# Kernel tuning notes

Hardware: AMD Instinct MI355X
Metric: run time of the kernel (lower is better)

The kernel has to match this reference:

```python
import jax, jax.numpy as jnp
import numpy as np

ALPHA = 0.2  # LeakyReLU negative slope
B, L, FIN, FOUT = 128, 512, 128, 128

def setup_inputs() -> dict:
    key = jax.random.key(0)
    k1, k2, k3, k4, k5 = jax.random.split(key, 5)
    h = jax.random.normal(k1, (B, L, FIN), jnp.float32)
    W = jax.random.normal(k2, (FIN, FOUT), jnp.float32) * (1.0 / np.sqrt(FIN))
    a = jax.random.normal(k3, (2 * FOUT,), jnp.float32) * (1.0 / np.sqrt(2 * FOUT))
    edge_bias = jax.random.normal(k4, (B, L, L), jnp.float32) * 0.1
    adj_mask = jax.random.uniform(k5, (L, L)) > 0.3
    adj_mask = adj_mask | jnp.eye(L, dtype=bool)  # self-loops avoid fully-masked rows
    return {"h": h, "W": W, "a": a, "edge_bias": edge_bias, "adj_mask": adj_mask}

def reference(h, W, a, edge_bias, adj_mask):
    # Wh: [B, L, Fout]
    Wh = jnp.einsum('blf,fo->blo', h, W)
    Fout = W.shape[1]
    # a([Wh_i, Wh_j]) == Wh_i @ a[:Fout] + Wh_j @ a[Fout:]  (avoids O(B*L*L*2F) concat)
    ei = Wh @ a[:Fout]   # [B, L]  (target i contribution)
    ej = Wh @ a[Fout:]   # [B, L]  (source j contribution)
    e = jax.nn.leaky_relu(ei[:, :, None] + ej[:, None, :], ALPHA) + edge_bias  # [B, L, L]
    e = jnp.where(adj_mask[None, :, :], e, -jnp.inf)
    att = jax.nn.softmax(e, axis=-1)  # dropout=0.0 -> identity
    h_prime = jnp.einsum('bij,bjo->bio', att, Wh)  # [B, L, Fout]
    return jax.nn.elu(h_prime)  # concat=True branch
```

## Files before the change

### kernel.cpp

```cpp
#include <hip/hip_runtime.h>
#include <string.h>

#define ALPHA 0.2f

typedef short short8 __attribute__((ext_vector_type(8)));
typedef float floatx4 __attribute__((ext_vector_type(4)));
typedef int intx4 __attribute__((ext_vector_type(4)));
typedef unsigned short ushort4v __attribute__((ext_vector_type(4)));

__device__ inline unsigned short f2bf(float f) {
    unsigned int v; __builtin_memcpy(&v, &f, 4);
    v = v + 0x7FFFu + ((v >> 16) & 1u);
    return (unsigned short)(v >> 16);
}

__global__ __launch_bounds__(256) void wh_kernel(const float* __restrict__ h,
                                                 const float* __restrict__ W,
                                                 const float* __restrict__ a,
                                                 unsigned short* __restrict__ wht,
                                                 float* __restrict__ ei,
                                                 float* __restrict__ ej)
{
    __shared__ __align__(16) unsigned short h_s[128][136];
    __shared__ __align__(16) unsigned short w_s[128][136];
    __shared__ float a_s[256];
    const int tid  = threadIdx.x;
    const int lane = tid & 63;
    const int wv   = tid >> 6;
    const int quad = lane >> 4;
    const int l16  = lane & 15;
    const int r0   = blockIdx.x * 128;
    const int b    = r0 >> 9;
    const int jb   = r0 & 511;

    const float* hbase = h + (size_t)r0 * 128;
    for (int it = 0; it < 16; ++it) {
        int idx4 = it * 256 + tid;
        floatx4 v = *(const floatx4*)(hbase + idx4 * 4);
        int row = idx4 >> 5;
        int col = (idx4 & 31) * 4;
        ushort4v u;
        for (int e = 0; e < 4; ++e) u[e] = f2bf(v[e]);
        *(ushort4v*)&h_s[row][col] = u;
    }
    for (int it = 0; it < 64; ++it) {
        int idx = it * 256 + tid;
        w_s[idx & 127][idx >> 7] = f2bf(W[idx]);
    }
    a_s[tid] = a[tid];
    __syncthreads();

    floatx4 acc[8][2];
    for (int mo = 0; mo < 8; ++mo)
        for (int n = 0; n < 2; ++n) acc[mo][n] = (floatx4)0.f;

    for (int kk = 0; kk < 4; ++kk) {
        short8 bfr[2];
        for (int n = 0; n < 2; ++n)
            bfr[n] = *(const short8*)&h_s[wv * 32 + n * 16 + l16][kk * 32 + quad * 8];
        for (int mo = 0; mo < 8; ++mo) {
            short8 afr = *(const short8*)&w_s[mo * 16 + l16][kk * 32 + quad * 8];
            acc[mo][0] = __builtin_amdgcn_mfma_f32_16x16x32_bf16(afr, bfr[0], acc[mo][0], 0, 0, 0);
            acc[mo][1] = __builtin_amdgcn_mfma_f32_16x16x32_bf16(afr, bfr[1], acc[mo][1], 0, 0, 0);
        }
    }

    for (int n = 0; n < 2; ++n) {
        float si = 0.f, sj = 0.f;
        for (int mo = 0; mo < 8; ++mo)
            for (int r = 0; r < 4; ++r) {
                int o = mo * 16 + quad * 4 + r;
                float v = acc[mo][n][r];
                si += v * a_s[o];
                sj += v * a_s[128 + o];
            }
        si += __shfl_xor(si, 16); si += __shfl_xor(si, 32);
        sj += __shfl_xor(sj, 16); sj += __shfl_xor(sj, 32);
        if (quad == 0) {
            int j = jb + wv * 32 + n * 16 + l16;
            ei[b * 512 + j] = si;
            ej[b * 512 + j] = sj;
        }
    }

    for (int mo = 0; mo < 8; ++mo)
        for (int n = 0; n < 2; ++n)
            for (int r = 0; r < 4; ++r) {
                int o = mo * 16 + quad * 4 + r;
                int j = jb + wv * 32 + n * 16 + l16;
                wht[(size_t)b * 65536 + o * 512 + j] = f2bf(acc[mo][n][r]);
            }
}

__global__ __launch_bounds__(256, 4) void attn_kernel(const unsigned short* __restrict__ wht,
                                                      const float* __restrict__ ei,
                                                      const float* __restrict__ ej,
                                                      const float* __restrict__ bias,
                                                      const int* __restrict__ adj,
                                                      float* __restrict__ out)
{
    __shared__ __align__(16) unsigned short p_s[32][520];
    __shared__ float ei_s[32];
    __shared__ float s_row[32];

    const int tid  = threadIdx.x;
    const int lane = tid & 63;
    const int wv   = tid >> 6;
    const int quad = lane >> 4;
    const int l16  = lane & 15;
    const int b    = blockIdx.x >> 4;
    const int i0   = (blockIdx.x & 15) * 32;

    const floatx4 ejv0 = *(const floatx4*)(ej + b * 512 + lane * 4);
    const floatx4 ejv1 = *(const floatx4*)(ej + b * 512 + 256 + lane * 4);
    if (tid < 32) ei_s[tid] = ei[b * 512 + i0 + tid];
    __syncthreads();

    const float* bp = bias + ((size_t)(b * 512 + i0 + wv * 8)) * 512;
    const int*   ap = adj + (i0 + wv * 8) * 512;
    floatx4 bb0 = *(const floatx4*)(bp + lane * 4);
    floatx4 bb1 = *(const floatx4*)(bp + 256 + lane * 4);
    intx4   mm0 = *(const intx4*)(ap + lane * 4);
    intx4   mm1 = *(const intx4*)(ap + 256 + lane * 4);

    float rsum[8];

#pragma unroll
    for (int rr = 0; rr < 8; ++rr) {
        floatx4 nb0, nb1; intx4 nm0, nm1;
        if (rr < 7) {
            nb0 = *(const floatx4*)(bp + 512 + lane * 4);
            nb1 = *(const floatx4*)(bp + 768 + lane * 4);
            nm0 = *(const intx4*)(ap + 512 + lane * 4);
            nm1 = *(const intx4*)(ap + 768 + lane * 4);
        }
        const int il = wv * 8 + rr;
        const float eiv = ei_s[il];
        float sm = 0.f;
        ushort4v p0, p1;
        for (int e = 0; e < 4; ++e) {
            float x = eiv + ejv0[e];
            x = fmaxf(x, ALPHA * x);
            x += bb0[e];
            float p = __expf(x);
            p = (mm0[e] != 0) ? p : 0.f;
            sm += p;
            p0[e] = f2bf(p);
        }
        for (int e = 0; e < 4; ++e) {
            float x = eiv + ejv1[e];
            x = fmaxf(x, ALPHA * x);
            x += bb1[e];
            float p = __expf(x);
            p = (mm1[e] != 0) ? p : 0.f;
            sm += p;
            p1[e] = f2bf(p);
        }
        *(ushort4v*)&p_s[il][lane * 4]       = p0;
        *(ushort4v*)&p_s[il][256 + lane * 4] = p1;
        rsum[rr] = sm;
        bb0 = nb0; bb1 = nb1; mm0 = nm0; mm1 = nm1;
        bp += 512; ap += 512;
    }

#pragma unroll
    for (int rr = 0; rr < 8; ++rr)
        for (int off = 32; off; off >>= 1)
            rsum[rr] += __shfl_xor(rsum[rr], off);
    if (lane == 0)
#pragma unroll
        for (int rr = 0; rr < 8; ++rr) s_row[wv * 8 + rr] = rsum[rr];
    __syncthreads();

    floatx4 acc[2][2];
    for (int m = 0; m < 2; ++m)
        for (int n = 0; n < 2; ++n) acc[m][n] = (floatx4)0.f;

    const unsigned short* wbase = wht + (size_t)b * 65536;
    const unsigned short* wb0 = wbase + (wv * 32 + l16) * 512 + quad * 8;
    const unsigned short* wb1 = wbase + (wv * 32 + 16 + l16) * 512 + quad * 8;
    short8 bf0 = *(const short8*)(wb0);
    short8 bf1 = *(const short8*)(wb1);
#pragma unroll
    for (int k16 = 0; k16 < 16; ++k16) {
        int ko = k16 * 32 + quad * 8;
        short8 nbf0, nbf1;
        if (k16 < 15) {
            nbf0 = *(const short8*)(wb0 + (k16 + 1) * 32);
            nbf1 = *(const short8*)(wb1 + (k16 + 1) * 32);
        }
        short8 af0 = *(const short8*)&p_s[l16][ko];
        short8 af1 = *(const short8*)&p_s[16 + l16][ko];
        acc[0][0] = __builtin_amdgcn_mfma_f32_16x16x32_bf16(af0, bf0, acc[0][0], 0, 0, 0);
        acc[0][1] = __builtin_amdgcn_mfma_f32_16x16x32_bf16(af0, bf1, acc[0][1], 0, 0, 0);
        acc[1][0] = __builtin_amdgcn_mfma_f32_16x16x32_bf16(af1, bf0, acc[1][0], 0, 0, 0);
        acc[1][1] = __builtin_amdgcn_mfma_f32_16x16x32_bf16(af1, bf1, acc[1][1], 0, 0, 0);
        bf0 = nbf0; bf1 = nbf1;
    }

    for (int m = 0; m < 2; ++m)
        for (int n = 0; n < 2; ++n)
            for (int r = 0; r < 4; ++r) {
                int il = m * 16 + quad * 4 + r;
                int o  = wv * 32 + n * 16 + l16;
                float v = acc[m][n][r] / s_row[il];
                v = v > 0.f ? v : (__expf(v) - 1.f);
                out[((size_t)(b * 512 + i0 + il)) * 128 + o] = v;
            }
}

extern "C" void kernel_launch(void* const* d_in, const int* in_sizes, int n_in,
                              void* d_out, int out_size, void* d_ws, size_t ws_size,
                              hipStream_t stream)
{
    const float* h    = (const float*)d_in[0];
    const float* W    = (const float*)d_in[1];
    const float* a    = (const float*)d_in[2];
    const float* bias = (const float*)d_in[3];
    const int*   adj  = (const int*)d_in[4];
    float*       out  = (float*)d_out;

    unsigned short* wht = (unsigned short*)d_ws;
    float* ei = (float*)((char*)d_ws + 16777216);
    float* ej = ei + 65536;

    hipLaunchKernelGGL(wh_kernel,   dim3(512),  dim3(256), 0, stream, h, W, a, wht, ei, ej);
    hipLaunchKernelGGL(attn_kernel, dim3(2048), dim3(256), 0, stream, wht, ei, ej, bias, adj, out);
}
```

Baseline: 262.3 us.

## Halve attention row tile, precompute bf16 mask, deepen Wh prefetch

Adds a small kernel that converts the int adjacency mask into a bf16 0/1 multiplier once per call, halving the mask bytes read by the attention kernel and replacing the select with a multiply. The attention kernel now processes 16 rows per block instead of 32, doubling the grid. It issues all bias and mask loads up front and prefetches Wh four k-steps ahead. The cost is that each Wh tile is now reloaded by twice as many blocks, plus an extra launch.

```diff
diff --git a/kernel.cpp b/kernel.cpp
--- a/kernel.cpp
+++ b/kernel.cpp
@@ -12,6 +12,13 @@
     unsigned int v; __builtin_memcpy(&v, &f, 4);
     v = v + 0x7FFFu + ((v >> 16) & 1u);
     return (unsigned short)(v >> 16);
+}
+
+__global__ __launch_bounds__(256) void mask_kernel(const int* __restrict__ adj,
+                                                   unsigned short* __restrict__ mbf)
+{
+    int idx = blockIdx.x * 256 + threadIdx.x;
+    mbf[idx] = adj[idx] ? (unsigned short)0x3F80 : (unsigned short)0;
 }
 
 __global__ __launch_bounds__(256) void wh_kernel(const float* __restrict__ h,
@@ -92,121 +99,117 @@
             }
 }
 
-__global__ __launch_bounds__(256, 4) void attn_kernel(const unsigned short* __restrict__ wht,
-                                                      const float* __restrict__ ei,
-                                                      const float* __restrict__ ej,
-                                                      const float* __restrict__ bias,
-                                                      const int* __restrict__ adj,
-                                                      float* __restrict__ out)
-{
-    __shared__ __align__(16) unsigned short p_s[32][520];
-    __shared__ float ei_s[32];
-    __shared__ float s_row[32];
+__global__ __launch_bounds__(256) void attn_kernel(const unsigned short* __restrict__ wht,
+                                                   const float* __restrict__ ei,
+                                                   const float* __restrict__ ej,
+                                                   const float* __restrict__ bias,
+                                                   const unsigned short* __restrict__ mbf,
+                                                   float* __restrict__ out)
+{
+    __shared__ __align__(16) unsigned short p_s[16][520];
+    __shared__ float ei_s[16];
+    __shared__ float s_row[16];
 
     const int tid  = threadIdx.x;
     const int lane = tid & 63;
     const int wv   = tid >> 6;
     const int quad = lane >> 4;
     const int l16  = lane & 15;
-    const int b    = blockIdx.x >> 4;
-    const int i0   = (blockIdx.x & 15) * 32;
-
+    const int b    = blockIdx.x >> 5;
+    const int i0   = (blockIdx.x & 31) * 16;
+
+    const float* bp = bias + ((size_t)(b * 512 + i0 + wv * 4)) * 512;
+    const unsigned short* mp = mbf + (i0 + wv * 4) * 512;
+    floatx4 b0[4], b1[4];
+    ushort4v m0[4], m1[4];
+#pragma unroll
+    for (int r = 0; r < 4; ++r) {
+        b0[r] = *(const floatx4*)(bp + r * 512 + lane * 4);
+        b1[r] = *(const floatx4*)(bp + r * 512 + 256 + lane * 4);
+        m0[r] = *(const ushort4v*)(mp + r * 512 + lane * 4);
+        m1[r] = *(const ushort4v*)(mp + r * 512 + 256 + lane * 4);
+    }
     const floatx4 ejv0 = *(const floatx4*)(ej + b * 512 + lane * 4);
     const floatx4 ejv1 = *(const floatx4*)(ej + b * 512 + 256 + lane * 4);
-    if (tid < 32) ei_s[tid] = ei[b * 512 + i0 + tid];
+    if (tid < 16) ei_s[tid] = ei[b * 512 + i0 + tid];
+
+    const unsigned short* wb0 = wht + (size_t)b * 65536 + (wv * 32 + l16) * 512 + quad * 8;
+    const unsigned short* wb1 = wb0 + 16 * 512;
+    short8 pb0[4], pb1[4];
+#pragma unroll
+    for (int s = 0; s < 4; ++s) {
+        pb0[s] = *(const short8*)(wb0 + s * 32);
+        pb1[s] = *(const short8*)(wb1 + s * 32);
+    }
     __syncthreads();
 
-    const float* bp = bias + ((size_t)(b * 512 + i0 + wv * 8)) * 512;
-    const int*   ap = adj + (i0 + wv * 8) * 512;
-    floatx4 bb0 = *(const floatx4*)(bp + lane * 4);
-    floatx4 bb1 = *(const floatx4*)(bp + 256 + lane * 4);
-    intx4   mm0 = *(const intx4*)(ap + lane * 4);
-    intx4   mm1 = *(const intx4*)(ap + 256 + lane * 4);
-
-    float rsum[8];
-
-#pragma unroll
-    for (int rr = 0; rr < 8; ++rr) {
-        floatx4 nb0, nb1; intx4 nm0, nm1;
-        if (rr < 7) {
-            nb0 = *(const floatx4*)(bp + 512 + lane * 4);
-            nb1 = *(const floatx4*)(bp + 768 + lane * 4);
-            nm0 = *(const intx4*)(ap + 512 + lane * 4);
-            nm1 = *(const intx4*)(ap + 768 + lane * 4);
-        }
-        const int il = wv * 8 + rr;
+    float rsum[4];
+#pragma unroll
+    for (int r = 0; r < 4; ++r) {
+        const int il = wv * 4 + r;
         const float eiv = ei_s[il];
-        float sm = 0.f;
-        ushort4v p0, p1;
+        float p[8];
+#pragma unroll
         for (int e = 0; e < 4; ++e) {
             float x = eiv + ejv0[e];
             x = fmaxf(x, ALPHA * x);
-            x += bb0[e];
-            float p = __expf(x);
-            p = (mm0[e] != 0) ? p : 0.f;
-            sm += p;
-            p0[e] = f2bf(p);
-        }
+            x += b0[r][e];
+            float mlt; { unsigned int mv = ((unsigned int)m0[r][e]) << 16; __builtin_memcpy(&mlt, &mv, 4); }
+            p[e] = __expf(x) * mlt;
+        }
+#pragma unroll
         for (int e = 0; e < 4; ++e) {
             float x = eiv + ejv1[e];
             x = fmaxf(x, ALPHA * x);
-            x += bb1[e];
-            float p = __expf(x);
-            p = (mm1[e] != 0) ? p : 0.f;
-            sm += p;
-            p1[e] = f2bf(p);
-        }
-        *(ushort4v*)&p_s[il][lane * 4]       = p0;
-        *(ushort4v*)&p_s[il][256 + lane * 4] = p1;
-        rsum[rr] = sm;
-        bb0 = nb0; bb1 = nb1; mm0 = nm0; mm1 = nm1;
-        bp += 512; ap += 512;
-    }
-
-#pragma unroll
-    for (int rr = 0; rr < 8; ++rr)
+            x += b1[r][e];
+            float mlt; { unsigned int mv = ((unsigned int)m1[r][e]) << 16; __builtin_memcpy(&mlt, &mv, 4); }
+            p[4 + e] = __expf(x) * mlt;
+        }
+        float sm = 0.f;
+#pragma unroll
+        for (int e = 0; e < 8; ++e) sm += p[e];
+        rsum[r] = sm;
+        ushort4v pk0, pk1;
+        for (int e = 0; e < 4; ++e) pk0[e] = f2bf(p[e]);
+        for (int e = 0; e < 4; ++e) pk1[e] = f2bf(p[4 + e]);
+        *(ushort4v*)&p_s[il][lane * 4]       = pk0;
+        *(ushort4v*)&p_s[il][256 + lane * 4] = pk1;
+    }
+#pragma unroll
+    for (int r = 0; r < 4; ++r)
         for (int off = 32; off; off >>= 1)
-            rsum[rr] += __shfl_xor(rsum[rr], off);
+            rsum[r] += __shfl_xor(rsum[r], off);
     if (lane == 0)
 #pragma unroll
-        for (int rr = 0; rr < 8; ++rr) s_row[wv * 8 + rr] = rsum[rr];
+        for (int r = 0; r < 4; ++r) s_row[wv * 4 + r] = rsum[r];
     __syncthreads();
 
-    floatx4 acc[2][2];
-    for (int m = 0; m < 2; ++m)
-        for (int n = 0; n < 2; ++n) acc[m][n] = (floatx4)0.f;
-
-    const unsigned short* wbase = wht + (size_t)b * 65536;
-    const unsigned short* wb0 = wbase + (wv * 32 + l16) * 512 + quad * 8;
-    const unsigned short* wb1 = wbase + (wv * 32 + 16 + l16) * 512 + quad * 8;
-    short8 bf0 = *(const short8*)(wb0);
-    short8 bf1 = *(const short8*)(wb1);
+    floatx4 acc0 = (floatx4)0.f, acc1 = (floatx4)0.f;
 #pragma unroll
     for (int k16 = 0; k16 < 16; ++k16) {
-        int ko = k16 * 32 + quad * 8;
-        short8 nbf0, nbf1;
-        if (k16 < 15) {
-            nbf0 = *(const short8*)(wb0 + (k16 + 1) * 32);
-            nbf1 = *(const short8*)(wb1 + (k16 + 1) * 32);
-        }
-        short8 af0 = *(const short8*)&p_s[l16][ko];
-        short8 af1 = *(const short8*)&p_s[16 + l16][ko];
-        acc[0][0] = __builtin_amdgcn_mfma_f32_16x16x32_bf16(af0, bf0, acc[0][0], 0, 0, 0);
-        acc[0][1] = __builtin_amdgcn_mfma_f32_16x16x32_bf16(af0, bf1, acc[0][1], 0, 0, 0);
-        acc[1][0] = __builtin_amdgcn_mfma_f32_16x16x32_bf16(af1, bf0, acc[1][0], 0, 0, 0);
-        acc[1][1] = __builtin_amdgcn_mfma_f32_16x16x32_bf16(af1, bf1, acc[1][1], 0, 0, 0);
-        bf0 = nbf0; bf1 = nbf1;
-    }
-
-    for (int m = 0; m < 2; ++m)
-        for (int n = 0; n < 2; ++n)
-            for (int r = 0; r < 4; ++r) {
-                int il = m * 16 + quad * 4 + r;
-                int o  = wv * 32 + n * 16 + l16;
-                float v = acc[m][n][r] / s_row[il];
-                v = v > 0.f ? v : (__expf(v) - 1.f);
-                out[((size_t)(b * 512 + i0 + il)) * 128 + o] = v;
-            }
+        short8 cur0 = pb0[k16 & 3];
+        short8 cur1 = pb1[k16 & 3];
+        if (k16 < 12) {
+            pb0[k16 & 3] = *(const short8*)(wb0 + (k16 + 4) * 32);
+            pb1[k16 & 3] = *(const short8*)(wb1 + (k16 + 4) * 32);
+        }
+        short8 af = *(const short8*)&p_s[l16][k16 * 32 + quad * 8];
+        acc0 = __builtin_amdgcn_mfma_f32_16x16x32_bf16(af, cur0, acc0, 0, 0, 0);
+        acc1 = __builtin_amdgcn_mfma_f32_16x16x32_bf16(af, cur1, acc1, 0, 0, 0);
+    }
+
+#pragma unroll
+    for (int r = 0; r < 4; ++r) {
+        int il = quad * 4 + r;
+        float inv = 1.f / s_row[il];
+        float v0 = acc0[r] * inv;
+        float v1 = acc1[r] * inv;
+        v0 = v0 > 0.f ? v0 : (__expf(v0) - 1.f);
+        v1 = v1 > 0.f ? v1 : (__expf(v1) - 1.f);
+        size_t base = ((size_t)(b * 512 + i0 + il)) * 128;
+        out[base + wv * 32 + l16]      = v0;
+        out[base + wv * 32 + 16 + l16] = v1;
+    }
 }
 
 extern "C" void kernel_launch(void* const* d_in, const int* in_sizes, int n_in,
@@ -223,7 +226,9 @@
     unsigned short* wht = (unsigned short*)d_ws;
     float* ei = (float*)((char*)d_ws + 16777216);
     float* ej = ei + 65536;
-
+    unsigned short* mbf = (unsigned short*)(ej + 65536);
+
+    hipLaunchKernelGGL(mask_kernel, dim3(1024), dim3(256), 0, stream, adj, mbf);
     hipLaunchKernelGGL(wh_kernel,   dim3(512),  dim3(256), 0, stream, h, W, a, wht, ei, ej);
-    hipLaunchKernelGGL(attn_kernel, dim3(2048), dim3(256), 0, stream, wht, ei, ej, bias, adj, out);
-}
+    hipLaunchKernelGGL(attn_kernel, dim3(4096), dim3(256), 0, stream, wht, ei, ej, bias, mbf, out);
+}
```

New measurement: 275.4 us. 5.0% more time.
